# Kernel optimization log

Hardware: AMD Instinct MI355X
Metric: run time of the kernel (lower is better)

The kernel has to match this reference:

```python
import jax, jax.numpy as jnp
import numpy as np

P_DROP = 0.2
N_NODES = 100000
N_EDGES = 1600000
IN_DIM, HID_DIM, OUT_DIM = 128, 128, 64


def sage_conv(x, src, dst, Wl, Wr, b, n_nodes):
    # PyG SAGEConv (aggr='mean', root_weight=True):
    #   out_i = W_l @ mean_{j in N(i)} x_j + W_r @ x_i + b
    msgs = jnp.take(x, src, axis=0)                                   # [E, d]
    agg = jax.ops.segment_sum(msgs, dst, num_segments=n_nodes)        # [N, d]
    cnt = jax.ops.segment_sum(jnp.ones((src.shape[0],), x.dtype), dst,
                              num_segments=n_nodes)                   # [N]
    agg = agg / jnp.maximum(cnt, 1.0)[:, None]                        # mean, 0 for isolated nodes
    return agg @ Wl + x @ Wr + b


def setup_inputs() -> dict:
    key = jax.random.key(0)
    ks = jax.random.split(key, 8)
    x = jax.random.normal(ks[0], (N_NODES, IN_DIM), dtype=jnp.float32)
    edge_index = jax.random.randint(ks[1], (2, N_EDGES), 0, N_NODES, dtype=jnp.int32)
    drop_u = jax.random.uniform(ks[2], (N_NODES, HID_DIM), dtype=jnp.float32)
    s1 = 1.0 / np.sqrt(IN_DIM)
    s2 = 1.0 / np.sqrt(HID_DIM)
    W1l = jax.random.normal(ks[3], (IN_DIM, HID_DIM), dtype=jnp.float32) * s1
    W1r = jax.random.normal(ks[4], (IN_DIM, HID_DIM), dtype=jnp.float32) * s1
    b1 = jnp.zeros((HID_DIM,), dtype=jnp.float32)
    W2l = jax.random.normal(ks[5], (HID_DIM, OUT_DIM), dtype=jnp.float32) * s2
    W2r = jax.random.normal(ks[6], (HID_DIM, OUT_DIM), dtype=jnp.float32) * s2
    b2 = jnp.zeros((OUT_DIM,), dtype=jnp.float32)
    return {"x": x, "edge_index": edge_index, "drop_u": drop_u,
            "W1l": W1l, "W1r": W1r, "b1": b1,
            "W2l": W2l, "W2r": W2r, "b2": b2}


def reference(x, edge_index, drop_u, W1l, W1r, b1, W2l, W2r, b2):
    n = x.shape[0]
    src, dst = edge_index[0], edge_index[1]
    h = jax.nn.elu(sage_conv(x, src, dst, W1l, W1r, b1, n))
    keep = (drop_u >= P_DROP).astype(h.dtype) / (1.0 - P_DROP)  # inverted dropout, p=0.2
    h = h * keep
    h = jax.nn.elu(sage_conv(h, src, dst, W2l, W2r, b2, n))
    return h
```

## Files before the change

kernel.cpp:

```cpp
#include <hip/hip_runtime.h>
#include <cstdint>
#include <cstddef>

#define TPB 256
#define BCAP 2560
#define NBKMAX 800
#define EPB 8192

typedef short bf16x8 __attribute__((ext_vector_type(8)));
typedef float f32x4 __attribute__((ext_vector_type(4)));

__device__ __forceinline__ unsigned short f2bf(float f) {
  unsigned int u = __float_as_uint(f);
  unsigned int r = (u + 0x7fffu + ((u >> 16) & 1u)) >> 16;
  return (unsigned short)r;
}
__device__ __forceinline__ float bf2f(unsigned short h) {
  return __uint_as_float(((unsigned int)h) << 16);
}

__device__ __forceinline__ float elu_neg(float v) { return __expf(v) - 1.0f; }

__device__ __forceinline__ void gload16(const void* g, void* l) {
  __builtin_amdgcn_global_load_lds(
      (const __attribute__((address_space(1))) unsigned int*)g,
      (__attribute__((address_space(3))) unsigned int*)l, 16, 0, 0);
}

template <int N>
__device__ __forceinline__ void waitvm() {
  asm volatile("s_waitcnt vmcnt(%0)" ::"n"(N) : "memory");
}


__global__ __launch_bounds__(256) void multisplit_scatter(
    const int* __restrict__ src, const int* __restrict__ dst,
    unsigned int* __restrict__ be, int* __restrict__ bcnt, int e, int nbk) {
  __shared__ int hist[NBKMAX];
  __shared__ int curs[NBKMAX];
  int tx = threadIdx.x;
  int e0 = blockIdx.x * EPB;
  int e1 = min(e, e0 + EPB);

  for (int b = tx; b < nbk; b += TPB) hist[b] = 0;
  __syncthreads();
  for (int i = e0 + tx; i < e1; i += TPB) atomicAdd(&hist[dst[i] >> 7], 1);
  __syncthreads();
  int rot = (blockIdx.x * 131) % nbk;
  for (int s = tx; s < nbk; s += TPB) {
    int b = s + rot;
    if (b >= nbk) b -= nbk;
    int h = hist[b];
    curs[b] = (h > 0) ? atomicAdd(&bcnt[b], h) : 0;
  }
  __syncthreads();
  for (int i = e0 + tx; i < e1; i += TPB) {
    int d = dst[i];
    int b = d >> 7;
    int p = atomicAdd(&curs[b], 1);
    if (p < BCAP)
      be[(size_t)b * BCAP + p] = ((unsigned int)(d & 127) << 17) | (unsigned int)src[i];
  }
}

__global__ __launch_bounds__(256) void per_bucket_build(
    const unsigned int* __restrict__ be, const int* __restrict__ bcnt,
    int* __restrict__ gcur, int* __restrict__ off, int* __restrict__ offend,
    int* __restrict__ col, int n) {
  int b = blockIdx.x, tx = threadIdx.x;
  int cnt = bcnt[b];
  if (cnt > BCAP) cnt = BCAP;
  int node0 = b << 7;
  __shared__ int scnt[128];
  __shared__ int sscan[128];
  __shared__ int sbase;
  if (tx < 128) scnt[tx] = 0;
  __syncthreads();
  const unsigned int* eb = be + (size_t)b * BCAP;
  for (int i = tx; i < cnt; i += 256) atomicAdd(&scnt[eb[i] >> 17], 1);
  __syncthreads();
  if (tx < 128) sscan[tx] = scnt[tx];
  __syncthreads();
  for (int d = 1; d < 128; d <<= 1) {
    int t = 0;
    if (tx < 128 && tx >= d) t = sscan[tx - d];
    __syncthreads();
    if (tx < 128) sscan[tx] += t;
    __syncthreads();
  }
  if (tx == 0) sbase = atomicAdd(gcur, cnt);
  __syncthreads();
  int base = sbase;
  if (tx < 128) {
    int excl = sscan[tx] - scnt[tx];
    if (node0 + tx < n) {
      off[node0 + tx] = base + excl;
      offend[node0 + tx] = base + sscan[tx];
    }
    scnt[tx] = excl;
  }
  __syncthreads();
  for (int i = tx; i < cnt; i += 256) {
    unsigned int u = eb[i];
    int p = atomicAdd(&scnt[u >> 17], 1);
    col[base + p] = (int)(u & 0x1ffff);
  }
}


__global__ void f32_to_bf16_v4(const float* __restrict__ in, unsigned short* __restrict__ out,
                               int n4) {
  int i = blockIdx.x * TPB + threadIdx.x;
  if (i >= n4) return;
  float4 v = ((const float4*)in)[i];
  ushort4 o;
  o.x = f2bf(v.x); o.y = f2bf(v.y); o.z = f2bf(v.z); o.w = f2bf(v.w);
  ((ushort4*)out)[i] = o;
}

__global__ void make_dropmask(const float* __restrict__ u, unsigned char* __restrict__ m,
                              int n4) {
  int i = blockIdx.x * TPB + threadIdx.x;
  if (i >= n4) return;
  float4 v = ((const float4*)u)[i];
  uchar4 o;
  o.x = (v.x >= 0.2f) ? 1 : 0;
  o.y = (v.y >= 0.2f) ? 1 : 0;
  o.z = (v.z >= 0.2f) ? 1 : 0;
  o.w = (v.w >= 0.2f) ? 1 : 0;
  ((uchar4*)m)[i] = o;
}

template <int NF>
__global__ void build_wt(const float* __restrict__ Wl, const float* __restrict__ Wr,
                         unsigned short* __restrict__ Wt) {
  int idx = blockIdx.x * TPB + threadIdx.x;
  if (idx >= NF * 256) return;
  int nn = idx >> 8;
  int k = idx & 255;
  float v = (k < 128) ? Wl[k * NF + nn] : Wr[(k - 128) * NF + nn];
  Wt[idx] = f2bf(v);
}

__global__ void build_wt2p(const float* __restrict__ W2l, const float* __restrict__ W2r,
                           unsigned short* __restrict__ Wt) {
  int idx = blockIdx.x * TPB + threadIdx.x;
  if (idx >= 128 * 128) return;
  int nn = idx >> 7;
  int k = idx & 127;
  float v = (nn < 64) ? W2l[k * 64 + nn] : W2r[k * 64 + (nn - 64)];
  Wt[idx] = f2bf(v);
}


__global__ void aggregate_bf(const unsigned short* __restrict__ X,
                             const int* __restrict__ off, const int* __restrict__ offend,
                             const int* __restrict__ col,
                             unsigned short* __restrict__ out, int n) {
  int wv = (blockIdx.x * TPB + threadIdx.x) >> 6;
  int lane = threadIdx.x & 63;
  int li = lane & 15;
  int node = wv * 4 + (lane >> 4);
  if (node >= n) return;
  int s0 = off[node], s1 = offend[node];
  int cnt = s1 - s0;

  float a0 = 0.f, a1 = 0.f, a2 = 0.f, a3 = 0.f,
        a4 = 0.f, a5 = 0.f, a6 = 0.f, a7 = 0.f;

  for (int base = 0; base < cnt; base += 16) {
    int idx = s0 + base + li;
    int ci = col[min(idx, s1 - 1)];
    int lim = cnt - base;
#pragma unroll
    for (int j = 0; j < 16; ++j) {
      int c = __shfl(ci, j, 16);
      const uint4* p = (const uint4*)(X + (size_t)c * 128 + li * 8);
      uint4 v = *p;
      float s = (j < lim) ? 1.f : 0.f;
      a0 = fmaf(s, __uint_as_float(v.x << 16), a0);
      a1 = fmaf(s, __uint_as_float(v.x & 0xffff0000u), a1);
      a2 = fmaf(s, __uint_as_float(v.y << 16), a2);
      a3 = fmaf(s, __uint_as_float(v.y & 0xffff0000u), a3);
      a4 = fmaf(s, __uint_as_float(v.z << 16), a4);
      a5 = fmaf(s, __uint_as_float(v.z & 0xffff0000u), a5);
      a6 = fmaf(s, __uint_as_float(v.w << 16), a6);
      a7 = fmaf(s, __uint_as_float(v.w & 0xffff0000u), a7);
    }
  }

  float inv = (cnt > 0) ? 1.0f / (float)cnt : 0.f;
  uint4 o;
  o.x = ((unsigned int)f2bf(a1 * inv) << 16) | f2bf(a0 * inv);
  o.y = ((unsigned int)f2bf(a3 * inv) << 16) | f2bf(a2 * inv);
  o.z = ((unsigned int)f2bf(a5 * inv) << 16) | f2bf(a4 * inv);
  o.w = ((unsigned int)f2bf(a7 * inv) << 16) | f2bf(a6 * inv);
  *(uint4*)(out + (size_t)node * 128 + li * 8) = o;
}


__global__ void aggregate_add(const unsigned short* __restrict__ P,
                              const int* __restrict__ off, const int* __restrict__ offend,
                              const int* __restrict__ col,
                              const float* __restrict__ Q, float* __restrict__ out, int n) {
  int wv = (blockIdx.x * TPB + threadIdx.x) >> 6;
  int lane = threadIdx.x & 63;
  int li = lane & 7;
  int node = wv * 8 + (lane >> 3);
  bool alive = node < n;
  int s0 = 0, s1 = 0;
  if (alive) { s0 = off[node]; s1 = offend[node]; }
  int cnt = s1 - s0;

  float a0 = 0.f, a1 = 0.f, a2 = 0.f, a3 = 0.f,
        a4 = 0.f, a5 = 0.f, a6 = 0.f, a7 = 0.f;

  for (int base = 0; base < cnt; base += 8) {
    int ci = col[max(0, min(s0 + base + li, s1 - 1))];
    int lim = cnt - base;
#pragma unroll
    for (int j = 0; j < 8; ++j) {
      int c = __shfl(ci, j, 8);
      uint4 v = *(const uint4*)(P + (size_t)c * 64 + li * 8);
      float s = (j < lim) ? 1.f : 0.f;
      a0 = fmaf(s, __uint_as_float(v.x << 16), a0);
      a1 = fmaf(s, __uint_as_float(v.x & 0xffff0000u), a1);
      a2 = fmaf(s, __uint_as_float(v.y << 16), a2);
      a3 = fmaf(s, __uint_as_float(v.y & 0xffff0000u), a3);
      a4 = fmaf(s, __uint_as_float(v.z << 16), a4);
      a5 = fmaf(s, __uint_as_float(v.z & 0xffff0000u), a5);
      a6 = fmaf(s, __uint_as_float(v.w << 16), a6);
      a7 = fmaf(s, __uint_as_float(v.w & 0xffff0000u), a7);
    }
  }

  if (alive) {
    float inv = (cnt > 0) ? 1.0f / (float)cnt : 0.f;
    const float4* qp = (const float4*)(Q + (size_t)node * 64 + li * 8);
    float4 q0 = qp[0], q1 = qp[1];
    float4 o0, o1;
    o0.x = a0 * inv + q0.x; o0.y = a1 * inv + q0.y;
    o0.z = a2 * inv + q0.z; o0.w = a3 * inv + q0.w;
    o1.x = a4 * inv + q1.x; o1.y = a5 * inv + q1.y;
    o1.z = a6 * inv + q1.z; o1.w = a7 * inv + q1.w;
    o0.x = (o0.x > 0.f) ? o0.x : elu_neg(o0.x);
    o0.y = (o0.y > 0.f) ? o0.y : elu_neg(o0.y);
    o0.z = (o0.z > 0.f) ? o0.z : elu_neg(o0.z);
    o0.w = (o0.w > 0.f) ? o0.w : elu_neg(o0.w);
    o1.x = (o1.x > 0.f) ? o1.x : elu_neg(o1.x);
    o1.y = (o1.y > 0.f) ? o1.y : elu_neg(o1.y);
    o1.z = (o1.z > 0.f) ? o1.z : elu_neg(o1.z);
    o1.w = (o1.w > 0.f) ? o1.w : elu_neg(o1.w);
    float4* op = (float4*)(out + (size_t)node * 64 + li * 8);
    op[0] = o0; op[1] = o1;
  }
}


template <int NCH, int MODE>
__global__ __launch_bounds__(256) void gemm_mfma(
    const unsigned short* __restrict__ A1, const unsigned short* __restrict__ A2,
    const unsigned short* __restrict__ Wt, const float* __restrict__ bias,
    const unsigned char* __restrict__ dmask, unsigned short* __restrict__ outb,
    float* __restrict__ outf, int n) {
  constexpr int IPC = 4;
  constexpr int KTOT = NCH * 64;
  __shared__ __align__(16) unsigned short sA[2][64 * 64];
  __shared__ __align__(16) unsigned short sB[2][64 * 64];

  int g = blockIdx.x;
  int p = (g >> 4) * 8 + (g & 7);
  int yy = (g >> 3) & 1;
  int nrb = (n + 63) >> 6;
  if (p >= nrb) return;

  int tid = threadIdx.x;
  int row0 = p * 64;
  int ncol0 = yy * 64;
  int lane = tid & 63;
  int wid = tid >> 6;
  int wm = wid >> 1, wn = wid & 1;
  int lq = lane & 15, q = lane >> 4;

  int sr = tid >> 3, sc8 = tid & 7;
  int cg = sc8 ^ (sr & 7);

  int arow[2];
#pragma unroll
  for (int t = 0; t < 2; ++t) arow[t] = min(row0 + sr + t * 32, n - 1);

  f32x4 acc[2][2];
#pragma unroll
  for (int i = 0; i < 2; ++i)
#pragma unroll
    for (int j = 0; j < 2; ++j) acc[i][j] = (f32x4)(0.f);

  auto issue = [&](int c, int b) {
    const unsigned short* Asrc = (MODE == 0 && c >= NCH / 2) ? A2 : A1;
    int koff = (MODE == 0 ? (c & (NCH / 2 - 1)) : c) * 64;
#pragma unroll
    for (int t = 0; t < 2; ++t) {
      gload16(Asrc + (size_t)arow[t] * 128 + koff + cg * 8,
              (char*)sA[b] + t * 4096 + wid * 1024);
    }
#pragma unroll
    for (int t = 0; t < 2; ++t) {
      gload16(Wt + (size_t)(ncol0 + sr + t * 32) * KTOT + c * 64 + cg * 8,
              (char*)sB[b] + t * 4096 + wid * 1024);
    }
  };

  issue(0, 0);
  issue(1, 1);

#pragma unroll
  for (int c = 0; c < NCH; ++c) {
    if (c < NCH - 1) waitvm<IPC>(); else waitvm<0>();
    __builtin_amdgcn_s_barrier();
    __builtin_amdgcn_sched_barrier(0);

    const int buf = c & 1;
#pragma unroll
    for (int ks = 0; ks < 2; ++ks) {
      bf16x8 a[2], b[2];
#pragma unroll
      for (int i = 0; i < 2; ++i) {
        int rr = wm * 32 + i * 16 + lq;
        a[i] = *(const bf16x8*)(&sA[buf][rr * 64 + (((ks * 4 + q) ^ (rr & 7)) * 8)]);
      }
#pragma unroll
      for (int j = 0; j < 2; ++j) {
        int rb = wn * 32 + j * 16 + lq;
        b[j] = *(const bf16x8*)(&sB[buf][rb * 64 + (((ks * 4 + q) ^ (rb & 7)) * 8)]);
      }
#pragma unroll
      for (int i = 0; i < 2; ++i)
#pragma unroll
        for (int j = 0; j < 2; ++j)
          acc[i][j] = __builtin_amdgcn_mfma_f32_16x16x32_bf16(a[i], b[j], acc[i][j], 0, 0, 0);
    }

    if (c < NCH - 2) {
      asm volatile("s_waitcnt lgkmcnt(0)" ::: "memory");
      __builtin_amdgcn_sched_barrier(0);
      __builtin_amdgcn_s_barrier();
      issue(c + 2, buf);
    }
  }

#pragma unroll
  for (int j = 0; j < 2; ++j) {
    int gcol = ncol0 + wn * 32 + j * 16 + lq;
    float bv;
    if (MODE == 0) bv = bias[gcol];
    else bv = (gcol >= 64) ? bias[gcol - 64] : 0.f;
#pragma unroll
    for (int i = 0; i < 2; ++i) {
      int rbase = row0 + wm * 32 + i * 16 + q * 4;
#pragma unroll
      for (int r = 0; r < 4; ++r) {
        int row = rbase + r;
        if (row >= n) continue;
        float v = acc[i][j][r] + bv;
        if (MODE == 0) {
          v = (v > 0.f) ? v : elu_neg(v);
          unsigned char k = dmask[(size_t)row * 128 + gcol];
          v = k ? v * 1.25f : 0.f;
          outb[(size_t)row * 128 + gcol] = f2bf(v);
        } else {
          if (gcol < 64) outb[(size_t)row * 64 + gcol] = f2bf(v);
          else outf[(size_t)row * 64 + (gcol - 64)] = v;
        }
      }
    }
  }
}


extern "C" void kernel_launch(void* const* d_in, const int* in_sizes, int n_in,
                              void* d_out, int out_size, void* d_ws, size_t ws_size,
                              hipStream_t stream) {
  const float* x = (const float*)d_in[0];
  const int* ei = (const int*)d_in[1];
  const float* dropu = (const float*)d_in[2];
  const float* W1l = (const float*)d_in[3];
  const float* W1r = (const float*)d_in[4];
  const float* b1 = (const float*)d_in[5];
  const float* W2l = (const float*)d_in[6];
  const float* W2r = (const float*)d_in[7];
  const float* b2 = (const float*)d_in[8];

  int n = in_sizes[0] / 128;
  int e = in_sizes[1] / 2;
  const int* src = ei;
  const int* dst = ei + e;
  float* out = (float*)d_out;

  char* w = (char*)d_ws;
  auto alloc = [&](size_t bytes) -> char* {
    char* p = w;
    w += (bytes + 255) & ~(size_t)255;
    return p;
  };
  int nbk = (n + 127) / 128;
  int* off = (int*)alloc((size_t)n * sizeof(int));
  int* offend = (int*)alloc((size_t)n * sizeof(int));
  int* col = (int*)alloc((size_t)e * sizeof(int));
  int* bcnt = (int*)alloc((size_t)(nbk + 1) * sizeof(int));
  int* gcur = bcnt + nbk;
  unsigned short* xb = (unsigned short*)alloc((size_t)n * 128 * 2);
  unsigned short* hb = (unsigned short*)alloc((size_t)n * 128 * 2);
  unsigned short* aggb = (unsigned short*)alloc((size_t)n * 128 * 2);
  unsigned char* dmask = (unsigned char*)alloc((size_t)n * 128);
  unsigned short* Wt1 = (unsigned short*)alloc(128 * 256 * 2);
  unsigned short* Wt2 = (unsigned short*)alloc(128 * 128 * 2);
  unsigned int* be = (unsigned int*)aggb;
  unsigned short* pb = xb;
  float* qf = (float*)aggb;

  hipMemsetAsync(bcnt, 0, (size_t)(nbk + 1) * sizeof(int), stream);

  int gMS = (e + EPB - 1) / EPB;
  multisplit_scatter<<<gMS, TPB, 0, stream>>>(src, dst, be, bcnt, e, nbk);
  per_bucket_build<<<nbk, TPB, 0, stream>>>(be, bcnt, gcur, off, offend, col, n);

  int n4 = n * 128 / 4;
  f32_to_bf16_v4<<<(n4 + TPB - 1) / TPB, TPB, 0, stream>>>(x, xb, n4);
  make_dropmask<<<(n4 + TPB - 1) / TPB, TPB, 0, stream>>>(dropu, dmask, n4);
  build_wt<128><<<(128 * 256 + TPB - 1) / TPB, TPB, 0, stream>>>(W1l, W1r, Wt1);
  build_wt2p<<<(128 * 128 + TPB - 1) / TPB, TPB, 0, stream>>>(W2l, W2r, Wt2);

  int gAgg1 = ((n + 3) / 4 * 64 + TPB - 1) / TPB;
  int gAgg2 = (n + 31) / 32;
  int gR = (n + 63) / 64;
  int gG = ((gR + 7) / 8) * 16;

  aggregate_bf<<<gAgg1, TPB, 0, stream>>>(xb, off, offend, col, aggb, n);
  gemm_mfma<4, 0><<<gG, TPB, 0, stream>>>(aggb, xb, Wt1, b1, dmask, hb, nullptr, n);

  gemm_mfma<2, 1><<<gG, TPB, 0, stream>>>(hb, nullptr, Wt2, b2, nullptr, pb, qf, n);
  aggregate_add<<<gAgg2, TPB, 0, stream>>>(pb, off, offend, col, qf, out, n);
}
```

Before: 382.2 us.

## Drop dropmask kernel, batch gather loads in aggregation kernels, add launch bounds

```diff
diff --git a/kernel.cpp b/kernel.cpp
--- a/kernel.cpp
+++ b/kernel.cpp
@@ -118,19 +118,6 @@
   ((ushort4*)out)[i] = o;
 }
 
-__global__ void make_dropmask(const float* __restrict__ u, unsigned char* __restrict__ m,
-                              int n4) {
-  int i = blockIdx.x * TPB + threadIdx.x;
-  if (i >= n4) return;
-  float4 v = ((const float4*)u)[i];
-  uchar4 o;
-  o.x = (v.x >= 0.2f) ? 1 : 0;
-  o.y = (v.y >= 0.2f) ? 1 : 0;
-  o.z = (v.z >= 0.2f) ? 1 : 0;
-  o.w = (v.w >= 0.2f) ? 1 : 0;
-  ((uchar4*)m)[i] = o;
-}
-
 template <int NF>
 __global__ void build_wt(const float* __restrict__ Wl, const float* __restrict__ Wr,
                          unsigned short* __restrict__ Wt) {
@@ -153,10 +140,11 @@
 }
 
 
-__global__ void aggregate_bf(const unsigned short* __restrict__ X,
-                             const int* __restrict__ off, const int* __restrict__ offend,
-                             const int* __restrict__ col,
-                             unsigned short* __restrict__ out, int n) {
+__global__ __launch_bounds__(256, 4) void aggregate_bf(
+    const unsigned short* __restrict__ X,
+    const int* __restrict__ off, const int* __restrict__ offend,
+    const int* __restrict__ col,
+    unsigned short* __restrict__ out, int n) {
   int wv = (blockIdx.x * TPB + threadIdx.x) >> 6;
   int lane = threadIdx.x & 63;
   int li = lane & 15;
@@ -165,27 +153,33 @@
   int s0 = off[node], s1 = offend[node];
   int cnt = s1 - s0;
 
+  const char* Xb = (const char*)X;
+  unsigned lioff = (unsigned)(li * 16);
+
   float a0 = 0.f, a1 = 0.f, a2 = 0.f, a3 = 0.f,
         a4 = 0.f, a5 = 0.f, a6 = 0.f, a7 = 0.f;
 
   for (int base = 0; base < cnt; base += 16) {
     int idx = s0 + base + li;
-    int ci = col[min(idx, s1 - 1)];
+    int myoff = col[min(idx, s1 - 1)] << 8;
     int lim = cnt - base;
+    uint4 v[16];
 #pragma unroll
     for (int j = 0; j < 16; ++j) {
-      int c = __shfl(ci, j, 16);
-      const uint4* p = (const uint4*)(X + (size_t)c * 128 + li * 8);
-      uint4 v = *p;
+      unsigned o = (unsigned)__shfl(myoff, j, 16) + lioff;
+      v[j] = *(const uint4*)(Xb + o);
+    }
+#pragma unroll
+    for (int j = 0; j < 16; ++j) {
       float s = (j < lim) ? 1.f : 0.f;
-      a0 = fmaf(s, __uint_as_float(v.x << 16), a0);
-      a1 = fmaf(s, __uint_as_float(v.x & 0xffff0000u), a1);
-      a2 = fmaf(s, __uint_as_float(v.y << 16), a2);
-      a3 = fmaf(s, __uint_as_float(v.y & 0xffff0000u), a3);
-      a4 = fmaf(s, __uint_as_float(v.z << 16), a4);
-      a5 = fmaf(s, __uint_as_float(v.z & 0xffff0000u), a5);
-      a6 = fmaf(s, __uint_as_float(v.w << 16), a6);
-      a7 = fmaf(s, __uint_as_float(v.w & 0xffff0000u), a7);
+      a0 = fmaf(s, __uint_as_float(v[j].x << 16), a0);
+      a1 = fmaf(s, __uint_as_float(v[j].x & 0xffff0000u), a1);
+      a2 = fmaf(s, __uint_as_float(v[j].y << 16), a2);
+      a3 = fmaf(s, __uint_as_float(v[j].y & 0xffff0000u), a3);
+      a4 = fmaf(s, __uint_as_float(v[j].z << 16), a4);
+      a5 = fmaf(s, __uint_as_float(v[j].z & 0xffff0000u), a5);
+      a6 = fmaf(s, __uint_as_float(v[j].w << 16), a6);
+      a7 = fmaf(s, __uint_as_float(v[j].w & 0xffff0000u), a7);
     }
   }
 
@@ -199,10 +193,11 @@
 }
 
 
-__global__ void aggregate_add(const unsigned short* __restrict__ P,
-                              const int* __restrict__ off, const int* __restrict__ offend,
-                              const int* __restrict__ col,
-                              const float* __restrict__ Q, float* __restrict__ out, int n) {
+__global__ __launch_bounds__(256, 4) void aggregate_add(
+    const unsigned short* __restrict__ P,
+    const int* __restrict__ off, const int* __restrict__ offend,
+    const int* __restrict__ col,
+    const float* __restrict__ Q, float* __restrict__ out, int n) {
   int wv = (blockIdx.x * TPB + threadIdx.x) >> 6;
   int lane = threadIdx.x & 63;
   int li = lane & 7;
@@ -212,25 +207,32 @@
   if (alive) { s0 = off[node]; s1 = offend[node]; }
   int cnt = s1 - s0;
 
+  const char* Pb = (const char*)P;
+  unsigned lioff = (unsigned)(li * 16);
+
   float a0 = 0.f, a1 = 0.f, a2 = 0.f, a3 = 0.f,
         a4 = 0.f, a5 = 0.f, a6 = 0.f, a7 = 0.f;
 
   for (int base = 0; base < cnt; base += 8) {
-    int ci = col[max(0, min(s0 + base + li, s1 - 1))];
+    int myoff = col[max(0, min(s0 + base + li, s1 - 1))] << 7;
     int lim = cnt - base;
+    uint4 v[8];
 #pragma unroll
     for (int j = 0; j < 8; ++j) {
-      int c = __shfl(ci, j, 8);
-      uint4 v = *(const uint4*)(P + (size_t)c * 64 + li * 8);
+      unsigned o = (unsigned)__shfl(myoff, j, 8) + lioff;
+      v[j] = *(const uint4*)(Pb + o);
+    }
+#pragma unroll
+    for (int j = 0; j < 8; ++j) {
       float s = (j < lim) ? 1.f : 0.f;
-      a0 = fmaf(s, __uint_as_float(v.x << 16), a0);
-      a1 = fmaf(s, __uint_as_float(v.x & 0xffff0000u), a1);
-      a2 = fmaf(s, __uint_as_float(v.y << 16), a2);
-      a3 = fmaf(s, __uint_as_float(v.y & 0xffff0000u), a3);
-      a4 = fmaf(s, __uint_as_float(v.z << 16), a4);
-      a5 = fmaf(s, __uint_as_float(v.z & 0xffff0000u), a5);
-      a6 = fmaf(s, __uint_as_float(v.w << 16), a6);
-      a7 = fmaf(s, __uint_as_float(v.w & 0xffff0000u), a7);
+      a0 = fmaf(s, __uint_as_float(v[j].x << 16), a0);
+      a1 = fmaf(s, __uint_as_float(v[j].x & 0xffff0000u), a1);
+      a2 = fmaf(s, __uint_as_float(v[j].y << 16), a2);
+      a3 = fmaf(s, __uint_as_float(v[j].y & 0xffff0000u), a3);
+      a4 = fmaf(s, __uint_as_float(v[j].z << 16), a4);
+      a5 = fmaf(s, __uint_as_float(v[j].z & 0xffff0000u), a5);
+      a6 = fmaf(s, __uint_as_float(v[j].w << 16), a6);
+      a7 = fmaf(s, __uint_as_float(v[j].w & 0xffff0000u), a7);
     }
   }
 
@@ -261,7 +263,7 @@
 __global__ __launch_bounds__(256) void gemm_mfma(
     const unsigned short* __restrict__ A1, const unsigned short* __restrict__ A2,
     const unsigned short* __restrict__ Wt, const float* __restrict__ bias,
-    const unsigned char* __restrict__ dmask, unsigned short* __restrict__ outb,
+    const float* __restrict__ drp, unsigned short* __restrict__ outb,
     float* __restrict__ outf, int n) {
   constexpr int IPC = 4;
   constexpr int KTOT = NCH * 64;
@@ -364,8 +366,8 @@
         float v = acc[i][j][r] + bv;
         if (MODE == 0) {
           v = (v > 0.f) ? v : elu_neg(v);
-          unsigned char k = dmask[(size_t)row * 128 + gcol];
-          v = k ? v * 1.25f : 0.f;
+          float u = drp[(size_t)row * 128 + gcol];
+          v = (u >= 0.2f) ? v * 1.25f : 0.f;
           outb[(size_t)row * 128 + gcol] = f2bf(v);
         } else {
           if (gcol < 64) outb[(size_t)row * 64 + gcol] = f2bf(v);
@@ -411,7 +413,6 @@
   unsigned short* xb = (unsigned short*)alloc((size_t)n * 128 * 2);
   unsigned short* hb = (unsigned short*)alloc((size_t)n * 128 * 2);
   unsigned short* aggb = (unsigned short*)alloc((size_t)n * 128 * 2);
-  unsigned char* dmask = (unsigned char*)alloc((size_t)n * 128);
   unsigned short* Wt1 = (unsigned short*)alloc(128 * 256 * 2);
   unsigned short* Wt2 = (unsigned short*)alloc(128 * 128 * 2);
   unsigned int* be = (unsigned int*)aggb;
@@ -426,7 +427,6 @@
 
   int n4 = n * 128 / 4;
   f32_to_bf16_v4<<<(n4 + TPB - 1) / TPB, TPB, 0, stream>>>(x, xb, n4);
-  make_dropmask<<<(n4 + TPB - 1) / TPB, TPB, 0, stream>>>(dropu, dmask, n4);
   build_wt<128><<<(128 * 256 + TPB - 1) / TPB, TPB, 0, stream>>>(W1l, W1r, Wt1);
   build_wt2p<<<(128 * 128 + TPB - 1) / TPB, TPB, 0, stream>>>(W2l, W2r, Wt2);
 
@@ -436,7 +436,7 @@
   int gG = ((gR + 7) / 8) * 16;
 
   aggregate_bf<<<gAgg1, TPB, 0, stream>>>(xb, off, offend, col, aggb, n);
-  gemm_mfma<4, 0><<<gG, TPB, 0, stream>>>(aggb, xb, Wt1, b1, dmask, hb, nullptr, n);
+  gemm_mfma<4, 0><<<gG, TPB, 0, stream>>>(aggb, xb, Wt1, b1, dropu, hb, nullptr, n);
 
   gemm_mfma<2, 1><<<gG, TPB, 0, stream>>>(hb, nullptr, Wt2, b2, nullptr, pb, qf, n);
   aggregate_add<<<gAgg2, TPB, 0, stream>>>(pb, off, offend, col, qf, out, n);
```

Result: no change. 380.7 us (-0.4%).

## Fuse prep kernels, read dropout uniforms in GEMM epilogue, stage CSR build in LDS

Applied to the files above, without the earlier changes.

```diff
diff --git a/kernel.cpp b/kernel.cpp
--- a/kernel.cpp
+++ b/kernel.cpp
@@ -71,13 +71,17 @@
   int cnt = bcnt[b];
   if (cnt > BCAP) cnt = BCAP;
   int node0 = b << 7;
+  __shared__ unsigned int stage[BCAP];
+  __shared__ int ssrc[BCAP];
   __shared__ int scnt[128];
   __shared__ int sscan[128];
   __shared__ int sbase;
   if (tx < 128) scnt[tx] = 0;
   __syncthreads();
   const unsigned int* eb = be + (size_t)b * BCAP;
-  for (int i = tx; i < cnt; i += 256) atomicAdd(&scnt[eb[i] >> 17], 1);
+  for (int i = tx; i < cnt; i += 256) stage[i] = eb[i];
+  __syncthreads();
+  for (int i = tx; i < cnt; i += 256) atomicAdd(&scnt[stage[i] >> 17], 1);
   __syncthreads();
   if (tx < 128) sscan[tx] = scnt[tx];
   __syncthreads();
@@ -101,55 +105,43 @@
   }
   __syncthreads();
   for (int i = tx; i < cnt; i += 256) {
-    unsigned int u = eb[i];
+    unsigned int u = stage[i];
     int p = atomicAdd(&scnt[u >> 17], 1);
-    col[base + p] = (int)(u & 0x1ffff);
-  }
-}
-
-
-__global__ void f32_to_bf16_v4(const float* __restrict__ in, unsigned short* __restrict__ out,
-                               int n4) {
-  int i = blockIdx.x * TPB + threadIdx.x;
-  if (i >= n4) return;
-  float4 v = ((const float4*)in)[i];
-  ushort4 o;
-  o.x = f2bf(v.x); o.y = f2bf(v.y); o.z = f2bf(v.z); o.w = f2bf(v.w);
-  ((ushort4*)out)[i] = o;
-}
-
-__global__ void make_dropmask(const float* __restrict__ u, unsigned char* __restrict__ m,
-                              int n4) {
-  int i = blockIdx.x * TPB + threadIdx.x;
-  if (i >= n4) return;
-  float4 v = ((const float4*)u)[i];
-  uchar4 o;
-  o.x = (v.x >= 0.2f) ? 1 : 0;
-  o.y = (v.y >= 0.2f) ? 1 : 0;
-  o.z = (v.z >= 0.2f) ? 1 : 0;
-  o.w = (v.w >= 0.2f) ? 1 : 0;
-  ((uchar4*)m)[i] = o;
-}
-
-template <int NF>
-__global__ void build_wt(const float* __restrict__ Wl, const float* __restrict__ Wr,
-                         unsigned short* __restrict__ Wt) {
+    ssrc[p] = (int)(u & 0x1ffff);
+  }
+  __syncthreads();
+  for (int i = tx; i < cnt; i += 256) col[base + i] = ssrc[i];
+}
+
+
+__global__ void prep_all(const float* __restrict__ x, const float* __restrict__ W1l,
+                         const float* __restrict__ W1r, const float* __restrict__ W2l,
+                         const float* __restrict__ W2r, unsigned short* __restrict__ xb,
+                         unsigned short* __restrict__ Wt1, unsigned short* __restrict__ Wt2,
+                         int n4) {
   int idx = blockIdx.x * TPB + threadIdx.x;
-  if (idx >= NF * 256) return;
-  int nn = idx >> 8;
-  int k = idx & 255;
-  float v = (k < 128) ? Wl[k * NF + nn] : Wr[(k - 128) * NF + nn];
-  Wt[idx] = f2bf(v);
-}
-
-__global__ void build_wt2p(const float* __restrict__ W2l, const float* __restrict__ W2r,
-                           unsigned short* __restrict__ Wt) {
-  int idx = blockIdx.x * TPB + threadIdx.x;
-  if (idx >= 128 * 128) return;
-  int nn = idx >> 7;
-  int k = idx & 127;
-  float v = (nn < 64) ? W2l[k * 64 + nn] : W2r[k * 64 + (nn - 64)];
-  Wt[idx] = f2bf(v);
+  if (idx < n4) {
+    float4 v = ((const float4*)x)[idx];
+    ushort4 o;
+    o.x = f2bf(v.x); o.y = f2bf(v.y); o.z = f2bf(v.z); o.w = f2bf(v.w);
+    ((ushort4*)xb)[idx] = o;
+    return;
+  }
+  int r = idx - n4;
+  if (r < 128 * 256) {
+    int nn = r >> 8;
+    int k = r & 255;
+    float v = (k < 128) ? W1l[k * 128 + nn] : W1r[(k - 128) * 128 + nn];
+    Wt1[r] = f2bf(v);
+    return;
+  }
+  r -= 128 * 256;
+  if (r < 128 * 128) {
+    int nn = r >> 7;
+    int k = r & 127;
+    float v = (nn < 64) ? W2l[k * 64 + nn] : W2r[k * 64 + (nn - 64)];
+    Wt2[r] = f2bf(v);
+  }
 }
 
 
@@ -261,7 +253,7 @@
 __global__ __launch_bounds__(256) void gemm_mfma(
     const unsigned short* __restrict__ A1, const unsigned short* __restrict__ A2,
     const unsigned short* __restrict__ Wt, const float* __restrict__ bias,
-    const unsigned char* __restrict__ dmask, unsigned short* __restrict__ outb,
+    const float* __restrict__ drp, unsigned short* __restrict__ outb,
     float* __restrict__ outf, int n) {
   constexpr int IPC = 4;
   constexpr int KTOT = NCH * 64;
@@ -364,8 +356,8 @@
         float v = acc[i][j][r] + bv;
         if (MODE == 0) {
           v = (v > 0.f) ? v : elu_neg(v);
-          unsigned char k = dmask[(size_t)row * 128 + gcol];
-          v = k ? v * 1.25f : 0.f;
+          float u = drp[(size_t)row * 128 + gcol];
+          v = (u >= 0.2f) ? v * 1.25f : 0.f;
           outb[(size_t)row * 128 + gcol] = f2bf(v);
         } else {
           if (gcol < 64) outb[(size_t)row * 64 + gcol] = f2bf(v);
@@ -411,7 +403,6 @@
   unsigned short* xb = (unsigned short*)alloc((size_t)n * 128 * 2);
   unsigned short* hb = (unsigned short*)alloc((size_t)n * 128 * 2);
   unsigned short* aggb = (unsigned short*)alloc((size_t)n * 128 * 2);
-  unsigned char* dmask = (unsigned char*)alloc((size_t)n * 128);
   unsigned short* Wt1 = (unsigned short*)alloc(128 * 256 * 2);
   unsigned short* Wt2 = (unsigned short*)alloc(128 * 128 * 2);
   unsigned int* be = (unsigned int*)aggb;
@@ -425,10 +416,9 @@
   per_bucket_build<<<nbk, TPB, 0, stream>>>(be, bcnt, gcur, off, offend, col, n);
 
   int n4 = n * 128 / 4;
-  f32_to_bf16_v4<<<(n4 + TPB - 1) / TPB, TPB, 0, stream>>>(x, xb, n4);
-  make_dropmask<<<(n4 + TPB - 1) / TPB, TPB, 0, stream>>>(dropu, dmask, n4);
-  build_wt<128><<<(128 * 256 + TPB - 1) / TPB, TPB, 0, stream>>>(W1l, W1r, Wt1);
-  build_wt2p<<<(128 * 128 + TPB - 1) / TPB, TPB, 0, stream>>>(W2l, W2r, Wt2);
+  int prepTot = n4 + 128 * 256 + 128 * 128;
+  prep_all<<<(prepTot + TPB - 1) / TPB, TPB, 0, stream>>>(x, W1l, W1r, W2l, W2r,
+                                                          xb, Wt1, Wt2, n4);
 
   int gAgg1 = ((n + 3) / 4 * 64 + TPB - 1) / TPB;
   int gAgg2 = (n + 31) / 32;
@@ -436,7 +426,7 @@
   int gG = ((gR + 7) / 8) * 16;
 
   aggregate_bf<<<gAgg1, TPB, 0, stream>>>(xb, off, offend, col, aggb, n);
-  gemm_mfma<4, 0><<<gG, TPB, 0, stream>>>(aggb, xb, Wt1, b1, dmask, hb, nullptr, n);
+  gemm_mfma<4, 0><<<gG, TPB, 0, stream>>>(aggb, xb, Wt1, b1, dropu, hb, nullptr, n);
 
   gemm_mfma<2, 1><<<gG, TPB, 0, stream>>>(hb, nullptr, Wt2, b2, nullptr, pb, qf, n);
   aggregate_add<<<gAgg2, TPB, 0, stream>>>(pb, off, offend, col, qf, out, n);
```

New measurement: 371.6 us. 2.8% less time.
